# Performance work log

Hardware: AMD Instinct MI355X
Metric: run time of the kernel (lower is better)

## Reference

```python
import jax, jax.numpy as jnp
import numpy as np

LOSS_IDX = jnp.array([0, 1])    # loss_indices from __init__
BASIS_IDX = jnp.array([0, 1])   # dtw_mapping_basis (x, y)


def _dtw_path(cost):
    """Classic DTW DP + backtrack on cost [N, M].
    Returns padded alignment path (a, b) of length N+M-1 with validity mask.
    DP is run as an anti-diagonal wavefront scan (L = N+M-1 steps)."""
    N, M = cost.shape
    L = N + M - 1
    inf = jnp.float32(jnp.inf)
    i_idx = jnp.arange(N)

    def diag_step(carry, k):
        prev1, prev2 = carry  # diagonals k-1 and k-2, indexed by row i
        j = k - i_idx
        valid = (j >= 0) & (j < M)
        c = cost[i_idx, jnp.clip(j, 0, M - 1)]
        up = jnp.concatenate([jnp.full((1,), inf), prev1[:-1]])  # D[i-1, j]
        dg = jnp.concatenate([jnp.full((1,), inf), prev2[:-1]])  # D[i-1, j-1]
        lf = prev1                                               # D[i, j-1]
        best = jnp.minimum(jnp.minimum(up, dg), lf)
        best = jnp.where(jnp.isinf(best), jnp.float32(0.0), best)  # (0,0) seed
        cur = jnp.where(valid, c + best, inf)
        return (cur, prev1), cur

    init = (jnp.full((N,), inf), jnp.full((N,), inf))
    _, diags = jax.lax.scan(diag_step, init, jnp.arange(L))  # [L, N]: D[i,j] = diags[i+j, i]

    def getD(i, j):
        ok = (i >= 0) & (j >= 0)
        return jnp.where(ok, diags[jnp.clip(i + j, 0, L - 1), jnp.clip(i, 0, N - 1)], inf)

    def bt_step(carry, _):
        i, j, done = carry
        emit_valid = jnp.logical_not(done)
        cand = jnp.stack([getD(i - 1, j - 1), getD(i - 1, j), getD(i, j - 1)])
        m = jnp.argmin(cand)  # 0: diag, 1: up, 2: left
        ni = jnp.where(m == 2, i, i - 1)
        nj = jnp.where(m == 1, j, j - 1)
        done2 = done | ((i == 0) & (j == 0))
        ni = jnp.where(done2, 0, ni)
        nj = jnp.where(done2, 0, nj)
        return (ni, nj, done2), (i, j, emit_valid)

    init_bt = (jnp.int32(N - 1), jnp.int32(M - 1), jnp.bool_(False))
    _, (a, b, valid) = jax.lax.scan(bt_step, init_bt, None, length=L)
    return a, b, valid


def _dtw_loss_single(pred, targ, subcoef):
    # DTW alignment is computed on detached (numpy in torch) basis coords.
    p = jax.lax.stop_gradient(pred)[:, BASIS_IDX]
    t = jax.lax.stop_gradient(targ)[:, BASIS_IDX]
    # euclidean pairwise distance cost [N, M]
    cost = jnp.sqrt(jnp.sum((p[:, None, :] - t[None, :, :]) ** 2, axis=-1))
    a, b, valid = _dtw_path(cost)
    d = jnp.abs(pred[a][:, LOSS_IDX] - targ[b][:, LOSS_IDX]) * subcoef  # [L, 2]
    return jnp.sum(d * valid[:, None].astype(d.dtype))


def setup_inputs() -> dict:
    key = jax.random.key(0)
    k1, k2 = jax.random.split(key)
    B, N, M, F = 32, 1024, 1024, 4
    preds = jax.random.normal(k1, (B, N, F), dtype=jnp.float32)
    targs = jax.random.normal(k2, (B, M, F), dtype=jnp.float32)
    subcoef = jnp.ones((2,), dtype=jnp.float32)
    return {"preds": preds, "targs": targs, "subcoef": subcoef}


def reference(preds, targs, subcoef):
    per_sample = jax.vmap(_dtw_loss_single, in_axes=(0, 0, None))(preds, targs, subcoef)
    return jnp.sum(per_sample)
```

## Files before the change

kernel.cpp:

```cpp
#include <hip/hip_runtime.h>
#include <math.h>

#define BATCH 32
#define NN 1024
#define MM 1024
#define RR 4
#define CC 4
#define LANES 64
#define NWAVE 4
#define TPB (MM / 4)
#define NSUP (TPB + LANES - 1)
#define LAG 72
#define TOT (NSUP + (NWAVE - 1) * LAG)
#define DEPTH 32
#define DEC_WORDS_PER_BATCH ((NN / 4) * (MM / 4))
#define DEC_BYTES ((size_t)BATCH * DEC_WORDS_PER_BATCH * 4)
#define REQ_WS DEC_BYTES
#define LPATH (NN + MM - 1)

__global__ void init_kernel(float* out) { out[0] = 0.0f; }

__device__ inline void bt_walk4(const unsigned* __restrict__ sdec, int roff,
                                int iLow, int& i, int& j, int& n,
                                unsigned* __restrict__ path)
{
    int ri = i >> 2, jc = j >> 2;
    unsigned w = sdec[(ri - roff) * 256 + jc];
    while (true) {
        const int base = (ri - roff) * 256 + jc;
        const unsigned wl = sdec[(jc > 0)    ? base - 1   : base];
        const unsigned wu = sdec[(ri > roff) ? base - 256 : base];
        const unsigned wd = sdec[(ri > roff && jc > 0) ? base - 257 : base];
        bool done = false, susp = false;
        while (true) {
            path[n++] = ((unsigned)i << 16) | (unsigned)j;
            if ((i | j) == 0) { done = true; break; }
            const unsigned m = (w >> (((i & 3) * 4 + (j & 3)) * 2)) & 3u;
            i -= (m != 2u); j -= (m != 1u);
            if (i < iLow) { susp = true; break; }
            if ((i >> 2) != ri || (j >> 2) != jc) break;
        }
        if (done || susp) break;
        const int nri = i >> 2, njc = j >> 2;
        w = (nri == ri) ? wl : ((njc == jc) ? wu : wd);
        ri = nri; jc = njc;
    }
}

__global__ __launch_bounds__(256, 1) void dtw_fused(
    const float* __restrict__ preds, const float* __restrict__ targs,
    const float* __restrict__ subcoef, unsigned* __restrict__ dec,
    float* __restrict__ out)
{
    const int b = blockIdx.x, t = threadIdx.x;
    const int l = t & 63, w = t >> 6;
    const float INF = __builtin_inff();

    __shared__ float pxA[NN], pyA[NN], txA[MM], tyA[MM];
    __shared__ float4 ring[NWAVE - 1][DEPTH];
    __shared__ unsigned sdec[128 * 256];
    __shared__ unsigned path[LPATH + 1];
    __shared__ int sI, sJ, sN;
    __shared__ float wsum[NWAVE];

    for (int it = 0; it < NN / 256; ++it) {
        const int idx = it * 256 + t;
        const float4 p4 = ((const float4*)preds)[(size_t)b * NN + idx];
        pxA[idx] = p4.x; pyA[idx] = p4.y;
        const float4 t4 = ((const float4*)targs)[(size_t)b * MM + idx];
        txA[idx] = t4.x; tyA[idx] = t4.y;
    }
    __syncthreads();

    const int i0 = (w << 8) + (l << 2);
    const float4 px4 = ((const float4*)pxA)[i0 >> 2];
    const float4 py4 = ((const float4*)pyA)[i0 >> 2];
    const float px[RR] = {px4.x, px4.y, px4.z, px4.w};
    const float py[RR] = {py4.x, py4.y, py4.z, py4.w};
    unsigned* __restrict__ decT =
        dec + (size_t)b * DEC_WORDS_PER_BATCH + (size_t)(i0 >> 2) * TPB;

    float Dp[RR], Dbot[CC], bv[CC];
    #pragma unroll
    for (int r = 0; r < RR; ++r) Dp[r] = INF;
    #pragma unroll
    for (int c = 0; c < CC; ++c) { Dbot[c] = INF; bv[c] = INF; }
    float bndRet = (w == 0 && l == 0) ? 0.0f : INF;
    float4 gcur = make_float4(INF, INF, INF, INF);
    float4 tx4 = ((const float4*)txA)[0], ty4 = ((const float4*)tyA)[0];

    for (int u = 0; u < TOT; ++u) {
        const int ul = u - LAG * w;
        if (l == 0) {
            const bool gb = (w > 0) && (ul >= 0) && (ul < TPB);
            bv[0] = gb ? gcur.x : INF; bv[1] = gb ? gcur.y : INF;
            bv[2] = gb ? gcur.z : INF; bv[3] = gb ? gcur.w : INF;
        }
        const bool act = (ul >= l) && (ul < l + TPB);
        if (act) {
            const int j0 = CC * (ul - l);
            const float cx[CC] = {tx4.x, tx4.y, tx4.z, tx4.w};
            const float cy[CC] = {ty4.x, ty4.y, ty4.z, ty4.w};
            float cost[RR][CC];
            #pragma unroll
            for (int c = 0; c < CC; ++c)
                #pragma unroll
                for (int r = 0; r < RR; ++r) {
                    const float dx = px[r] - cx[c], dy = py[r] - cy[c];
                    cost[r][c] = __builtin_amdgcn_sqrtf(dx * dx + dy * dy);
                }
            unsigned word = 0;
            #pragma unroll
            for (int c = 0; c < CC; ++c) {
                float up = bv[c];
                float dg = (c == 0) ? bndRet : bv[c - 1];
                #pragma unroll
                for (int r = 0; r < RR; ++r) {
                    const float lf = Dp[r];
                    const unsigned m = (dg <= up && dg <= lf) ? 0u
                                     : ((up <= lf) ? 1u : 2u);
                    const float D = cost[r][c] + fminf(dg, fminf(up, lf));
                    word |= m << ((r * 4 + c) * 2);
                    dg = lf; up = D; Dp[r] = D;
                }
                Dbot[c] = up;
            }
            decT[j0 >> 2] = word;
            if (l == LANES - 1 && w < NWAVE - 1)
                ring[w][ul & (DEPTH - 1)] =
                    make_float4(Dbot[0], Dbot[1], Dbot[2], Dbot[3]);
        }
        bndRet = bv[CC - 1];
        #pragma unroll
        for (int c = 0; c < CC; ++c) bv[c] = __shfl_up(Dbot[c], 1);
        const int un = ul + 1;
        if (un >= l && un < l + TPB) {
            const int jn = CC * (un - l);
            tx4 = ((const float4*)txA)[jn >> 2];
            ty4 = ((const float4*)tyA)[jn >> 2];
        }
        if (l == 0 && w > 0 && un >= 0 && un < TPB)
            gcur = ring[w - 1][(un + 63) & (DEPTH - 1)];
        if ((u & 7) == 7) __syncthreads();
    }

    __threadfence_block();
    __syncthreads();

    const unsigned* __restrict__ decB = dec + (size_t)b * DEC_WORDS_PER_BATCH;
    {
        uint4* s4 = (uint4*)sdec;
        const uint4* g4 = (const uint4*)(decB + 128 * 256);
        for (int k = t; k < 8192; k += 256) s4[k] = g4[k];
    }
    __syncthreads();
    if (t == 0) {
        int i = NN - 1, j = MM - 1, n = 0;
        bt_walk4(sdec, 128, 512, i, j, n, path);
        sI = i; sJ = j; sN = n;
    }
    __syncthreads();
    {
        uint4* s4 = (uint4*)sdec;
        const uint4* g4 = (const uint4*)decB;
        for (int k = t; k < 8192; k += 256) s4[k] = g4[k];
    }
    __syncthreads();
    if (t == 0) {
        int i = sI, j = sJ, n = sN;
        bt_walk4(sdec, 0, 0, i, j, n, path);
        sN = n;
    }
    __syncthreads();

    const float sc0 = subcoef[0], sc1 = subcoef[1];
    const int n = sN;
    float acc = 0.0f;
    for (int p = t; p < n; p += 256) {
        const unsigned e = path[p];
        const int i = (int)(e >> 16), j = (int)(e & 0xffffu);
        acc += fabsf(pxA[i] - txA[j]) * sc0 + fabsf(pyA[i] - tyA[j]) * sc1;
    }
    #pragma unroll
    for (int o = 32; o > 0; o >>= 1) acc += __shfl_down(acc, o);
    if ((t & 63) == 0) wsum[t >> 6] = acc;
    __syncthreads();
    if (t == 0) atomicAdd(out, (wsum[0] + wsum[1]) + (wsum[2] + wsum[3]));
}

__global__ __launch_bounds__(256) void dtw_fallback(
    const float* __restrict__ preds, const float* __restrict__ targs,
    const float* __restrict__ subcoef, unsigned* __restrict__ dec,
    float* __restrict__ out)
{
    const int b = blockIdx.x;
    const int t = threadIdx.x;
    const float INF = __builtin_inff();
    __shared__ float px[NN], py[NN];
    __shared__ float txy[2 * MM];
    __shared__ float bbuf[2][256];

    for (int it = 0; it < NN / 256; ++it) {
        const int idx = it * 256 + t;
        const float4 p4 = ((const float4*)preds)[(size_t)b * NN + idx];
        px[idx] = p4.x; py[idx] = p4.y;
        const float4 t4 = ((const float4*)targs)[(size_t)b * MM + idx];
        txy[2 * idx] = t4.x; txy[2 * idx + 1] = t4.y;
    }
    bbuf[0][t] = INF; bbuf[1][t] = INF;
    __syncthreads();

    float pxr[4], pyr[4], Dp[4];
    #pragma unroll
    for (int r = 0; r < 4; ++r) {
        pxr[r] = px[4 * t + r]; pyr[r] = py[4 * t + r]; Dp[r] = INF;
    }
    float dgB = (t == 0) ? 0.0f : INF;
    unsigned packed = 0;
    unsigned* decB = dec + (size_t)b * 65536;
    for (int s = 0; s < MM + 255; ++s) {
        const int j = s - t;
        const float upB = (t == 0) ? INF : bbuf[(s + 1) & 1][t - 1];
        if (j >= 0 && j < MM) {
            const float txj = txy[2 * j], tyj = txy[2 * j + 1];
            float up = upB, dg = dgB;
            unsigned mbits = 0;
            #pragma unroll
            for (int r = 0; r < 4; ++r) {
                const float dx = pxr[r] - txj, dy = pyr[r] - tyj;
                const float c = sqrtf(dx * dx + dy * dy);
                const float lf = Dp[r];
                const unsigned m = (dg <= up && dg <= lf) ? 0u
                                 : ((up <= lf) ? 1u : 2u);
                mbits |= m << (r * 8 + (j & 3) * 2);
                const float Dc = c + fminf(up, fminf(dg, lf));
                dg = lf; up = Dc; Dp[r] = Dc;
            }
            packed |= mbits;
            if ((j & 3) == 3) { decB[(unsigned)t * 256 + (j >> 2)] = packed; packed = 0; }
            bbuf[s & 1][t] = Dp[3];
        }
        dgB = upB;
        __syncthreads();
    }
    __threadfence_block();
    __syncthreads();
    if (t == 0) {
        const float sc0 = subcoef[0], sc1 = subcoef[1];
        int i = NN - 1, jj = MM - 1;
        float loss = 0.0f;
        int ti = i >> 2, tj = jj >> 2;
        unsigned wv = decB[ti * 256 + tj];
        while (true) {
            const int tjl = (tj > 0) ? tj - 1 : 0;
            const int til = (ti > 0) ? ti - 1 : 0;
            const unsigned wl = decB[ti * 256 + tjl];
            const unsigned wu = decB[til * 256 + tj];
            const unsigned wd = decB[til * 256 + tjl];
            bool done = false;
            while (true) {
                loss += fabsf(px[i] - txy[2 * jj]) * sc0
                      + fabsf(py[i] - txy[2 * jj + 1]) * sc1;
                if ((i | jj) == 0) { done = true; break; }
                const unsigned m = (wv >> (((i & 3) * 4 + (jj & 3)) * 2)) & 3u;
                i -= (m != 2u); jj -= (m != 1u);
                if ((i >> 2) != ti || (jj >> 2) != tj) break;
            }
            if (done) break;
            const int nti = i >> 2, ntj = jj >> 2;
            wv = (nti == ti) ? wl : ((ntj == tj) ? wu : wd);
            ti = nti; tj = ntj;
        }
        atomicAdd(out, loss);
    }
}

extern "C" void kernel_launch(void* const* d_in, const int* in_sizes, int n_in,
                              void* d_out, int out_size, void* d_ws, size_t ws_size,
                              hipStream_t stream) {
    const float* preds   = (const float*)d_in[0];
    const float* targs   = (const float*)d_in[1];
    const float* subcoef = (const float*)d_in[2];
    float* out = (float*)d_out;
    unsigned* dec = (unsigned*)d_ws;

    init_kernel<<<1, 1, 0, stream>>>(out);
    if (ws_size >= REQ_WS) {
        dtw_fused<<<BATCH, 256, 0, stream>>>(preds, targs, subcoef, dec, out);
    } else {
        dtw_fallback<<<BATCH, 256, 0, stream>>>(preds, targs, subcoef, dec, out);
    }
}
```

Before: 597.1 us.

## Interleave two DP wavefront roles per wave in a 128-thread block

The block shrinks from four waves to two. Each wave now advances two independent row-band DP chains (roles w and w+2) in the same loop iteration, through a shared per-step helper. The aim is to expose instruction-level parallelism that hides the latency of the serial per-step dependency chain, including the cross-lane permute, which is now done with ds_bpermute instead of __shfl_up. The cost is that each SIMD now issues twice the instructions and holds twice the register state, and the final reduction and shared-memory copies are remapped to the smaller block.

```diff
diff --git a/kernel.cpp b/kernel.cpp
--- a/kernel.cpp
+++ b/kernel.cpp
@@ -47,7 +47,77 @@
     }
 }
 
-__global__ __launch_bounds__(256, 1) void dtw_fused(
+struct SS {
+    float Dp[RR], Dbot[CC], bv[CC], bndRet;
+    float px[RR], py[RR];
+    float4 tx4, ty4, gcur;
+    unsigned* decT;
+};
+
+__device__ __forceinline__ void dp_step(SS& S, const int u, const int role,
+                                        const int l, const int bpa,
+                                        const float* __restrict__ txA,
+                                        const float* __restrict__ tyA,
+                                        float4* __restrict__ ringW,
+                                        const float4* __restrict__ ringR)
+{
+    const float INF = __builtin_inff();
+    const int ul = u - LAG * role;
+    if (l == 0) {
+        const bool gb = (role > 0) && (ul >= 0) && (ul < TPB);
+        S.bv[0] = gb ? S.gcur.x : INF; S.bv[1] = gb ? S.gcur.y : INF;
+        S.bv[2] = gb ? S.gcur.z : INF; S.bv[3] = gb ? S.gcur.w : INF;
+    }
+    const bool act = (ul >= l) && (ul < l + TPB);
+    if (act) {
+        const int j0 = CC * (ul - l);
+        const float cx[CC] = {S.tx4.x, S.tx4.y, S.tx4.z, S.tx4.w};
+        const float cy[CC] = {S.ty4.x, S.ty4.y, S.ty4.z, S.ty4.w};
+        float cost[RR][CC];
+        #pragma unroll
+        for (int c = 0; c < CC; ++c)
+            #pragma unroll
+            for (int r = 0; r < RR; ++r) {
+                const float dx = S.px[r] - cx[c], dy = S.py[r] - cy[c];
+                cost[r][c] = __builtin_amdgcn_sqrtf(dx * dx + dy * dy);
+            }
+        unsigned word = 0;
+        #pragma unroll
+        for (int c = 0; c < CC; ++c) {
+            float up = S.bv[c];
+            float dg = (c == 0) ? S.bndRet : S.bv[c - 1];
+            #pragma unroll
+            for (int r = 0; r < RR; ++r) {
+                const float lf = S.Dp[r];
+                const unsigned m = (dg <= up && dg <= lf) ? 0u
+                                 : ((up <= lf) ? 1u : 2u);
+                const float D = cost[r][c] + fminf(dg, fminf(up, lf));
+                word |= m << ((r * 4 + c) * 2);
+                dg = lf; up = D; S.Dp[r] = D;
+            }
+            S.Dbot[c] = up;
+        }
+        S.decT[j0 >> 2] = word;
+        if (l == LANES - 1 && role < NWAVE - 1)
+            ringW[ul & (DEPTH - 1)] =
+                make_float4(S.Dbot[0], S.Dbot[1], S.Dbot[2], S.Dbot[3]);
+    }
+    S.bndRet = S.bv[CC - 1];
+    #pragma unroll
+    for (int c = 0; c < CC; ++c)
+        S.bv[c] = __int_as_float(
+            __builtin_amdgcn_ds_bpermute(bpa, __float_as_int(S.Dbot[c])));
+    const int un = ul + 1;
+    if (un >= l && un < l + TPB) {
+        const int jn = CC * (un - l);
+        S.tx4 = ((const float4*)txA)[jn >> 2];
+        S.ty4 = ((const float4*)tyA)[jn >> 2];
+    }
+    if (l == 0 && role > 0 && un >= 0 && un < TPB)
+        S.gcur = ringR[(un + 63) & (DEPTH - 1)];
+}
+
+__global__ __launch_bounds__(128, 1) void dtw_fused(
     const float* __restrict__ preds, const float* __restrict__ targs,
     const float* __restrict__ subcoef, unsigned* __restrict__ dec,
     float* __restrict__ out)
@@ -63,8 +133,8 @@
     __shared__ int sI, sJ, sN;
     __shared__ float wsum[NWAVE];
 
-    for (int it = 0; it < NN / 256; ++it) {
-        const int idx = it * 256 + t;
+    for (int it = 0; it < NN / 128; ++it) {
+        const int idx = it * 128 + t;
         const float4 p4 = ((const float4*)preds)[(size_t)b * NN + idx];
         pxA[idx] = p4.x; pyA[idx] = p4.y;
         const float4 t4 = ((const float4*)targs)[(size_t)b * MM + idx];
@@ -72,75 +142,45 @@
     }
     __syncthreads();
 
-    const int i0 = (w << 8) + (l << 2);
-    const float4 px4 = ((const float4*)pxA)[i0 >> 2];
-    const float4 py4 = ((const float4*)pyA)[i0 >> 2];
-    const float px[RR] = {px4.x, px4.y, px4.z, px4.w};
-    const float py[RR] = {py4.x, py4.y, py4.z, py4.w};
-    unsigned* __restrict__ decT =
-        dec + (size_t)b * DEC_WORDS_PER_BATCH + (size_t)(i0 >> 2) * TPB;
-
-    float Dp[RR], Dbot[CC], bv[CC];
-    #pragma unroll
-    for (int r = 0; r < RR; ++r) Dp[r] = INF;
-    #pragma unroll
-    for (int c = 0; c < CC; ++c) { Dbot[c] = INF; bv[c] = INF; }
-    float bndRet = (w == 0 && l == 0) ? 0.0f : INF;
-    float4 gcur = make_float4(INF, INF, INF, INF);
-    float4 tx4 = ((const float4*)txA)[0], ty4 = ((const float4*)tyA)[0];
+    const int bpa = (l - 1) << 2;
+    const int roleA = w, roleB = w + 2;
+    SS A, B;
+    {
+        const int i0a = (roleA << 8) + (l << 2);
+        const int i0b = (roleB << 8) + (l << 2);
+        const float4 pxa = ((const float4*)pxA)[i0a >> 2];
+        const float4 pya = ((const float4*)pyA)[i0a >> 2];
+        const float4 pxb = ((const float4*)pxA)[i0b >> 2];
+        const float4 pyb = ((const float4*)pyA)[i0b >> 2];
+        A.px[0] = pxa.x; A.px[1] = pxa.y; A.px[2] = pxa.z; A.px[3] = pxa.w;
+        A.py[0] = pya.x; A.py[1] = pya.y; A.py[2] = pya.z; A.py[3] = pya.w;
+        B.px[0] = pxb.x; B.px[1] = pxb.y; B.px[2] = pxb.z; B.px[3] = pxb.w;
+        B.py[0] = pyb.x; B.py[1] = pyb.y; B.py[2] = pyb.z; B.py[3] = pyb.w;
+        A.decT = dec + (size_t)b * DEC_WORDS_PER_BATCH + (size_t)(i0a >> 2) * TPB;
+        B.decT = dec + (size_t)b * DEC_WORDS_PER_BATCH + (size_t)(i0b >> 2) * TPB;
+    }
+    #pragma unroll
+    for (int r = 0; r < RR; ++r) { A.Dp[r] = INF; B.Dp[r] = INF; }
+    #pragma unroll
+    for (int c = 0; c < CC; ++c) {
+        A.Dbot[c] = INF; A.bv[c] = INF;
+        B.Dbot[c] = INF; B.bv[c] = INF;
+    }
+    A.bndRet = (roleA == 0 && l == 0) ? 0.0f : INF;
+    B.bndRet = INF;
+    A.gcur = make_float4(INF, INF, INF, INF);
+    B.gcur = make_float4(INF, INF, INF, INF);
+    A.tx4 = ((const float4*)txA)[0]; A.ty4 = ((const float4*)tyA)[0];
+    B.tx4 = ((const float4*)txA)[0]; B.ty4 = ((const float4*)tyA)[0];
+
+    float4* ringWA = ring[roleA];
+    const float4* ringRA = ring[(w > 0) ? (roleA - 1) : 0];
+    float4* ringWB = ring[(w == 0) ? 2 : 0];
+    const float4* ringRB = ring[roleB - 1];
 
     for (int u = 0; u < TOT; ++u) {
-        const int ul = u - LAG * w;
-        if (l == 0) {
-            const bool gb = (w > 0) && (ul >= 0) && (ul < TPB);
-            bv[0] = gb ? gcur.x : INF; bv[1] = gb ? gcur.y : INF;
-            bv[2] = gb ? gcur.z : INF; bv[3] = gb ? gcur.w : INF;
-        }
-        const bool act = (ul >= l) && (ul < l + TPB);
-        if (act) {
-            const int j0 = CC * (ul - l);
-            const float cx[CC] = {tx4.x, tx4.y, tx4.z, tx4.w};
-            const float cy[CC] = {ty4.x, ty4.y, ty4.z, ty4.w};
-            float cost[RR][CC];
-            #pragma unroll
-            for (int c = 0; c < CC; ++c)
-                #pragma unroll
-                for (int r = 0; r < RR; ++r) {
-                    const float dx = px[r] - cx[c], dy = py[r] - cy[c];
-                    cost[r][c] = __builtin_amdgcn_sqrtf(dx * dx + dy * dy);
-                }
-            unsigned word = 0;
-            #pragma unroll
-            for (int c = 0; c < CC; ++c) {
-                float up = bv[c];
-                float dg = (c == 0) ? bndRet : bv[c - 1];
-                #pragma unroll
-                for (int r = 0; r < RR; ++r) {
-                    const float lf = Dp[r];
-                    const unsigned m = (dg <= up && dg <= lf) ? 0u
-                                     : ((up <= lf) ? 1u : 2u);
-                    const float D = cost[r][c] + fminf(dg, fminf(up, lf));
-                    word |= m << ((r * 4 + c) * 2);
-                    dg = lf; up = D; Dp[r] = D;
-                }
-                Dbot[c] = up;
-            }
-            decT[j0 >> 2] = word;
-            if (l == LANES - 1 && w < NWAVE - 1)
-                ring[w][ul & (DEPTH - 1)] =
-                    make_float4(Dbot[0], Dbot[1], Dbot[2], Dbot[3]);
-        }
-        bndRet = bv[CC - 1];
-        #pragma unroll
-        for (int c = 0; c < CC; ++c) bv[c] = __shfl_up(Dbot[c], 1);
-        const int un = ul + 1;
-        if (un >= l && un < l + TPB) {
-            const int jn = CC * (un - l);
-            tx4 = ((const float4*)txA)[jn >> 2];
-            ty4 = ((const float4*)tyA)[jn >> 2];
-        }
-        if (l == 0 && w > 0 && un >= 0 && un < TPB)
-            gcur = ring[w - 1][(un + 63) & (DEPTH - 1)];
+        dp_step(A, u, roleA, l, bpa, txA, tyA, ringWA, ringRA);
+        dp_step(B, u, roleB, l, bpa, txA, tyA, ringWB, ringRB);
         if ((u & 7) == 7) __syncthreads();
     }
 
@@ -151,7 +191,7 @@
     {
         uint4* s4 = (uint4*)sdec;
         const uint4* g4 = (const uint4*)(decB + 128 * 256);
-        for (int k = t; k < 8192; k += 256) s4[k] = g4[k];
+        for (int k = t; k < 8192; k += 128) s4[k] = g4[k];
     }
     __syncthreads();
     if (t == 0) {
@@ -163,7 +203,7 @@
     {
         uint4* s4 = (uint4*)sdec;
         const uint4* g4 = (const uint4*)decB;
-        for (int k = t; k < 8192; k += 256) s4[k] = g4[k];
+        for (int k = t; k < 8192; k += 128) s4[k] = g4[k];
     }
     __syncthreads();
     if (t == 0) {
@@ -175,15 +215,19 @@
 
     const float sc0 = subcoef[0], sc1 = subcoef[1];
     const int n = sN;
-    float acc = 0.0f;
-    for (int p = t; p < n; p += 256) {
-        const unsigned e = path[p];
-        const int i = (int)(e >> 16), j = (int)(e & 0xffffu);
-        acc += fabsf(pxA[i] - txA[j]) * sc0 + fabsf(pyA[i] - tyA[j]) * sc1;
-    }
-    #pragma unroll
-    for (int o = 32; o > 0; o >>= 1) acc += __shfl_down(acc, o);
-    if ((t & 63) == 0) wsum[t >> 6] = acc;
+    #pragma unroll
+    for (int po = 0; po < 2; ++po) {
+        const int ow = 2 * w + po;
+        float acc = 0.0f;
+        for (int p = 64 * ow + l; p < n; p += 256) {
+            const unsigned e = path[p];
+            const int i = (int)(e >> 16), j = (int)(e & 0xffffu);
+            acc += fabsf(pxA[i] - txA[j]) * sc0 + fabsf(pyA[i] - tyA[j]) * sc1;
+        }
+        #pragma unroll
+        for (int o = 32; o > 0; o >>= 1) acc += __shfl_down(acc, o);
+        if (l == 0) wsum[ow] = acc;
+    }
     __syncthreads();
     if (t == 0) atomicAdd(out, (wsum[0] + wsum[1]) + (wsum[2] + wsum[3]));
 }
@@ -286,7 +330,7 @@
 
     init_kernel<<<1, 1, 0, stream>>>(out);
     if (ws_size >= REQ_WS) {
-        dtw_fused<<<BATCH, 256, 0, stream>>>(preds, targs, subcoef, dec, out);
+        dtw_fused<<<BATCH, 128, 0, stream>>>(preds, targs, subcoef, dec, out);
     } else {
         dtw_fallback<<<BATCH, 256, 0, stream>>>(preds, targs, subcoef, dec, out);
     }
```

Result: slower. 803.2 us (+34.5%).

## Store DTW decision words in wavefront-coalesced layout and unswizzle on load

Applied to the files above, without the earlier changes.

During the wavefront DP each lane used to write its decision word to a row-major address, so the 64 lanes of a wave wrote strided locations. The new layout indexes words by (wave, step mod 256, lane), so each wave's store per step is contiguous and coalesced. The backtrack staging now unswizzles into the old row-major shared layout, with scattered LDS writes and extra index arithmetic. All lanes now also read the ring buffer through a hoisted pointer, not just lane 0, which removes a lane branch but adds redundant LDS reads.

```diff
diff --git a/kernel.cpp b/kernel.cpp
--- a/kernel.cpp
+++ b/kernel.cpp
@@ -77,8 +77,8 @@
     const float4 py4 = ((const float4*)pyA)[i0 >> 2];
     const float px[RR] = {px4.x, px4.y, px4.z, px4.w};
     const float py[RR] = {py4.x, py4.y, py4.z, py4.w};
-    unsigned* __restrict__ decT =
-        dec + (size_t)b * DEC_WORDS_PER_BATCH + (size_t)(i0 >> 2) * TPB;
+    unsigned* __restrict__ decW =
+        dec + (size_t)b * DEC_WORDS_PER_BATCH + ((size_t)w << 14) + (size_t)l;
 
     float Dp[RR], Dbot[CC], bv[CC];
     #pragma unroll
@@ -88,6 +88,7 @@
     float bndRet = (w == 0 && l == 0) ? 0.0f : INF;
     float4 gcur = make_float4(INF, INF, INF, INF);
     float4 tx4 = ((const float4*)txA)[0], ty4 = ((const float4*)tyA)[0];
+    const float4* __restrict__ ringR = ring[(w > 0) ? (w - 1) : 0];
 
     for (int u = 0; u < TOT; ++u) {
         const int ul = u - LAG * w;
@@ -98,7 +99,6 @@
         }
         const bool act = (ul >= l) && (ul < l + TPB);
         if (act) {
-            const int j0 = CC * (ul - l);
             const float cx[CC] = {tx4.x, tx4.y, tx4.z, tx4.w};
             const float cy[CC] = {ty4.x, ty4.y, ty4.z, ty4.w};
             float cost[RR][CC];
@@ -125,7 +125,7 @@
                 }
                 Dbot[c] = up;
             }
-            decT[j0 >> 2] = word;
+            decW[(ul & 255) << 6] = word;
             if (l == LANES - 1 && w < NWAVE - 1)
                 ring[w][ul & (DEPTH - 1)] =
                     make_float4(Dbot[0], Dbot[1], Dbot[2], Dbot[3]);
@@ -139,8 +139,8 @@
             tx4 = ((const float4*)txA)[jn >> 2];
             ty4 = ((const float4*)tyA)[jn >> 2];
         }
-        if (l == 0 && w > 0 && un >= 0 && un < TPB)
-            gcur = ring[w - 1][(un + 63) & (DEPTH - 1)];
+        if (w > 0 && un >= 0 && un < TPB)
+            gcur = ringR[(un + 63) & (DEPTH - 1)];
         if ((u & 7) == 7) __syncthreads();
     }
 
@@ -149,9 +149,23 @@
 
     const unsigned* __restrict__ decB = dec + (size_t)b * DEC_WORDS_PER_BATCH;
     {
-        uint4* s4 = (uint4*)sdec;
-        const uint4* g4 = (const uint4*)(decB + 128 * 256);
-        for (int k = t; k < 8192; k += 256) s4[k] = g4[k];
+        const uint4* g4 = (const uint4*)(decB + 32768);
+        for (int k = t; k < 8192; k += 256) {
+            const uint4 v = g4[k];
+            const int kb = k << 2;
+            const int wv = kb >> 14;
+            const int rem = kb & 16383;
+            const int q = rem >> 6;
+            const int lb = rem & 63;
+            const unsigned wd[4] = {v.x, v.y, v.z, v.w};
+            #pragma unroll
+            for (int e = 0; e < 4; ++e) {
+                const int ll = lb + e;
+                const int row = (wv << 6) + ll;
+                const int jc = (q - ll) & 255;
+                sdec[(row << 8) + jc] = wd[e];
+            }
+        }
     }
     __syncthreads();
     if (t == 0) {
@@ -161,9 +175,23 @@
     }
     __syncthreads();
     {
-        uint4* s4 = (uint4*)sdec;
         const uint4* g4 = (const uint4*)decB;
-        for (int k = t; k < 8192; k += 256) s4[k] = g4[k];
+        for (int k = t; k < 8192; k += 256) {
+            const uint4 v = g4[k];
+            const int kb = k << 2;
+            const int wv = kb >> 14;
+            const int rem = kb & 16383;
+            const int q = rem >> 6;
+            const int lb = rem & 63;
+            const unsigned wd[4] = {v.x, v.y, v.z, v.w};
+            #pragma unroll
+            for (int e = 0; e < 4; ++e) {
+                const int ll = lb + e;
+                const int row = (wv << 6) + ll;
+                const int jc = (q - ll) & 255;
+                sdec[(row << 8) + jc] = wd[e];
+            }
+        }
     }
     __syncthreads();
     if (t == 0) {
```

New measurement: 608.9 us. Within noise of the previous version (+2.0%).

## Use single-wave 16x8 register tiles for the DTW wavefront and drop inter-wave ring

Applied to the files above, without the earlier changes.

Replaces the four-wave pipelined wavefront (4x4 tiles per lane, shared-memory ring hand-off and periodic block barriers) with a single 64-lane wave where each lane owns 16 rows and computes 8 columns per step. The number of serial wavefront steps falls from about 535 to 191 and the per-step __syncthreads disappears. Each lane now does 128 cells of dependent min/add per step, so the per-step critical path grows. The direction-word layout changes to column-major pairs so each lane writes two uint4 stores, and the backtrack addressing is updated to match. The shared-memory copies and the final reduction now run with only 64 threads.

```diff
diff --git a/kernel.cpp b/kernel.cpp
--- a/kernel.cpp
+++ b/kernel.cpp
@@ -4,15 +4,11 @@
 #define BATCH 32
 #define NN 1024
 #define MM 1024
-#define RR 4
-#define CC 4
+#define RR 16
+#define CC 8
 #define LANES 64
-#define NWAVE 4
-#define TPB (MM / 4)
-#define NSUP (TPB + LANES - 1)
-#define LAG 72
-#define TOT (NSUP + (NWAVE - 1) * LAG)
-#define DEPTH 32
+#define TPB (MM / CC)
+#define TOT (TPB + LANES - 1)
 #define DEC_WORDS_PER_BATCH ((NN / 4) * (MM / 4))
 #define DEC_BYTES ((size_t)BATCH * DEC_WORDS_PER_BATCH * 4)
 #define REQ_WS DEC_BYTES
@@ -20,17 +16,19 @@
 
 __global__ void init_kernel(float* out) { out[0] = 0.0f; }
 
-__device__ inline void bt_walk4(const unsigned* __restrict__ sdec, int roff,
+__device__ inline void bt_walkP(const unsigned* __restrict__ sdec, int riOff,
                                 int iLow, int& i, int& j, int& n,
                                 unsigned* __restrict__ path)
 {
     int ri = i >> 2, jc = j >> 2;
-    unsigned w = sdec[(ri - roff) * 256 + jc];
+#define WADDR(R, C) (((((C) >> 1)) << 8) + (((R) - riOff) << 1) + ((C) & 1))
+    unsigned w = sdec[WADDR(ri, jc)];
     while (true) {
-        const int base = (ri - roff) * 256 + jc;
-        const unsigned wl = sdec[(jc > 0)    ? base - 1   : base];
-        const unsigned wu = sdec[(ri > roff) ? base - 256 : base];
-        const unsigned wd = sdec[(ri > roff && jc > 0) ? base - 257 : base];
+        const int riu = (ri > riOff) ? ri - 1 : ri;
+        const int jcl = (jc > 0) ? jc - 1 : jc;
+        const unsigned wl = sdec[WADDR(ri, jcl)];
+        const unsigned wu = sdec[WADDR(riu, jc)];
+        const unsigned wd = sdec[WADDR(riu, jcl)];
         bool done = false, susp = false;
         while (true) {
             path[n++] = ((unsigned)i << 16) | (unsigned)j;
@@ -45,26 +43,24 @@
         w = (nri == ri) ? wl : ((njc == jc) ? wu : wd);
         ri = nri; jc = njc;
     }
-}
-
-__global__ __launch_bounds__(256, 1) void dtw_fused(
+#undef WADDR
+}
+
+__global__ __launch_bounds__(64, 1) void dtw_fused(
     const float* __restrict__ preds, const float* __restrict__ targs,
     const float* __restrict__ subcoef, unsigned* __restrict__ dec,
     float* __restrict__ out)
 {
-    const int b = blockIdx.x, t = threadIdx.x;
-    const int l = t & 63, w = t >> 6;
+    const int b = blockIdx.x, l = threadIdx.x;
     const float INF = __builtin_inff();
 
     __shared__ float pxA[NN], pyA[NN], txA[MM], tyA[MM];
-    __shared__ float4 ring[NWAVE - 1][DEPTH];
-    __shared__ unsigned sdec[128 * 256];
+    __shared__ unsigned sdec[32768];
     __shared__ unsigned path[LPATH + 1];
     __shared__ int sI, sJ, sN;
-    __shared__ float wsum[NWAVE];
-
-    for (int it = 0; it < NN / 256; ++it) {
-        const int idx = it * 256 + t;
+
+    for (int it = 0; it < NN / 64; ++it) {
+        const int idx = it * 64 + l;
         const float4 p4 = ((const float4*)preds)[(size_t)b * NN + idx];
         pxA[idx] = p4.x; pyA[idx] = p4.y;
         const float4 t4 = ((const float4*)targs)[(size_t)b * MM + idx];
@@ -72,76 +68,70 @@
     }
     __syncthreads();
 
-    const int i0 = (w << 8) + (l << 2);
-    const float4 px4 = ((const float4*)pxA)[i0 >> 2];
-    const float4 py4 = ((const float4*)pyA)[i0 >> 2];
-    const float px[RR] = {px4.x, px4.y, px4.z, px4.w};
-    const float py[RR] = {py4.x, py4.y, py4.z, py4.w};
-    unsigned* __restrict__ decT =
-        dec + (size_t)b * DEC_WORDS_PER_BATCH + (size_t)(i0 >> 2) * TPB;
-
-    float Dp[RR], Dbot[CC], bv[CC];
+    float px[RR], py[RR];
+    #pragma unroll
+    for (int k = 0; k < 4; ++k) {
+        const float4 p4 = ((const float4*)pxA)[4 * l + k];
+        px[4 * k] = p4.x; px[4 * k + 1] = p4.y; px[4 * k + 2] = p4.z; px[4 * k + 3] = p4.w;
+        const float4 q4 = ((const float4*)pyA)[4 * l + k];
+        py[4 * k] = q4.x; py[4 * k + 1] = q4.y; py[4 * k + 2] = q4.z; py[4 * k + 3] = q4.w;
+    }
+    unsigned* __restrict__ decW = dec + (size_t)b * DEC_WORDS_PER_BATCH
+                                + ((size_t)(l >> 5) << 15) + ((size_t)(l & 31) << 3);
+
+    float Dp[RR], bv[CC], bot[CC];
     #pragma unroll
     for (int r = 0; r < RR; ++r) Dp[r] = INF;
     #pragma unroll
-    for (int c = 0; c < CC; ++c) { Dbot[c] = INF; bv[c] = INF; }
-    float bndRet = (w == 0 && l == 0) ? 0.0f : INF;
-    float4 gcur = make_float4(INF, INF, INF, INF);
-    float4 tx4 = ((const float4*)txA)[0], ty4 = ((const float4*)tyA)[0];
-
+    for (int c = 0; c < CC; ++c) { bv[c] = INF; bot[c] = INF; }
+    float bndRet = (l == 0) ? 0.0f : INF;
+    float4 tx0 = ((const float4*)txA)[0], tx1 = ((const float4*)txA)[1];
+    float4 ty0 = ((const float4*)tyA)[0], ty1 = ((const float4*)tyA)[1];
+
+    #pragma unroll 1
     for (int u = 0; u < TOT; ++u) {
-        const int ul = u - LAG * w;
-        if (l == 0) {
-            const bool gb = (w > 0) && (ul >= 0) && (ul < TPB);
-            bv[0] = gb ? gcur.x : INF; bv[1] = gb ? gcur.y : INF;
-            bv[2] = gb ? gcur.z : INF; bv[3] = gb ? gcur.w : INF;
-        }
-        const bool act = (ul >= l) && (ul < l + TPB);
+        const int q = u - l;
+        const bool act = (q >= 0) && (q < TPB);
         if (act) {
-            const int j0 = CC * (ul - l);
-            const float cx[CC] = {tx4.x, tx4.y, tx4.z, tx4.w};
-            const float cy[CC] = {ty4.x, ty4.y, ty4.z, ty4.w};
-            float cost[RR][CC];
-            #pragma unroll
-            for (int c = 0; c < CC; ++c)
-                #pragma unroll
-                for (int r = 0; r < RR; ++r) {
-                    const float dx = px[r] - cx[c], dy = py[r] - cy[c];
-                    cost[r][c] = __builtin_amdgcn_sqrtf(dx * dx + dy * dy);
-                }
-            unsigned word = 0;
+            const float cx[CC] = {tx0.x, tx0.y, tx0.z, tx0.w,
+                                  tx1.x, tx1.y, tx1.z, tx1.w};
+            const float cy[CC] = {ty0.x, ty0.y, ty0.z, ty0.w,
+                                  ty1.x, ty1.y, ty1.z, ty1.w};
+            unsigned wd[8] = {0, 0, 0, 0, 0, 0, 0, 0};
             #pragma unroll
             for (int c = 0; c < CC; ++c) {
                 float up = bv[c];
                 float dg = (c == 0) ? bndRet : bv[c - 1];
                 #pragma unroll
                 for (int r = 0; r < RR; ++r) {
+                    const float dx = px[r] - cx[c], dy = py[r] - cy[c];
+                    const float cost = __builtin_amdgcn_sqrtf(dx * dx + dy * dy);
                     const float lf = Dp[r];
-                    const unsigned m = (dg <= up && dg <= lf) ? 0u
-                                     : ((up <= lf) ? 1u : 2u);
-                    const float D = cost[r][c] + fminf(dg, fminf(up, lf));
-                    word |= m << ((r * 4 + c) * 2);
+                    const float mn = fminf(dg, fminf(up, lf));
+                    const unsigned m = (mn == dg) ? 0u : ((mn == up) ? 1u : 2u);
+                    wd[(r >> 2) * 2 + (c >> 2)] |= m << (((r & 3) * 4 + (c & 3)) * 2);
+                    const float D = cost + mn;
                     dg = lf; up = D; Dp[r] = D;
                 }
-                Dbot[c] = up;
+                bot[c] = up;
             }
-            decT[j0 >> 2] = word;
-            if (l == LANES - 1 && w < NWAVE - 1)
-                ring[w][ul & (DEPTH - 1)] =
-                    make_float4(Dbot[0], Dbot[1], Dbot[2], Dbot[3]);
+            uint4* dst = (uint4*)(decW + ((size_t)q << 8));
+            dst[0] = make_uint4(wd[0], wd[1], wd[2], wd[3]);
+            dst[1] = make_uint4(wd[4], wd[5], wd[6], wd[7]);
         }
         bndRet = bv[CC - 1];
         #pragma unroll
-        for (int c = 0; c < CC; ++c) bv[c] = __shfl_up(Dbot[c], 1);
-        const int un = ul + 1;
-        if (un >= l && un < l + TPB) {
-            const int jn = CC * (un - l);
-            tx4 = ((const float4*)txA)[jn >> 2];
-            ty4 = ((const float4*)tyA)[jn >> 2];
-        }
-        if (l == 0 && w > 0 && un >= 0 && un < TPB)
-            gcur = ring[w - 1][(un + 63) & (DEPTH - 1)];
-        if ((u & 7) == 7) __syncthreads();
+        for (int c = 0; c < CC; ++c) {
+            bv[c] = __shfl_up(bot[c], 1);
+            if (l == 0) bv[c] = INF;
+        }
+        const int qn = u + 1 - l;
+        if (qn >= 0 && qn < TPB) {
+            tx0 = ((const float4*)txA)[2 * qn];
+            tx1 = ((const float4*)txA)[2 * qn + 1];
+            ty0 = ((const float4*)tyA)[2 * qn];
+            ty1 = ((const float4*)tyA)[2 * qn + 1];
+        }
     }
 
     __threadfence_block();
@@ -149,26 +139,26 @@
 
     const unsigned* __restrict__ decB = dec + (size_t)b * DEC_WORDS_PER_BATCH;
     {
+        const uint4* g4 = (const uint4*)(decB + 32768);
         uint4* s4 = (uint4*)sdec;
-        const uint4* g4 = (const uint4*)(decB + 128 * 256);
-        for (int k = t; k < 8192; k += 256) s4[k] = g4[k];
-    }
-    __syncthreads();
-    if (t == 0) {
+        for (int k = l; k < 8192; k += 64) s4[k] = g4[k];
+    }
+    __syncthreads();
+    if (l == 0) {
         int i = NN - 1, j = MM - 1, n = 0;
-        bt_walk4(sdec, 128, 512, i, j, n, path);
+        bt_walkP(sdec, 128, 512, i, j, n, path);
         sI = i; sJ = j; sN = n;
     }
     __syncthreads();
     {
+        const uint4* g4 = (const uint4*)decB;
         uint4* s4 = (uint4*)sdec;
-        const uint4* g4 = (const uint4*)decB;
-        for (int k = t; k < 8192; k += 256) s4[k] = g4[k];
-    }
-    __syncthreads();
-    if (t == 0) {
+        for (int k = l; k < 8192; k += 64) s4[k] = g4[k];
+    }
+    __syncthreads();
+    if (l == 0) {
         int i = sI, j = sJ, n = sN;
-        bt_walk4(sdec, 0, 0, i, j, n, path);
+        bt_walkP(sdec, 0, 0, i, j, n, path);
         sN = n;
     }
     __syncthreads();
@@ -176,16 +166,14 @@
     const float sc0 = subcoef[0], sc1 = subcoef[1];
     const int n = sN;
     float acc = 0.0f;
-    for (int p = t; p < n; p += 256) {
+    for (int p = l; p < n; p += 64) {
         const unsigned e = path[p];
         const int i = (int)(e >> 16), j = (int)(e & 0xffffu);
         acc += fabsf(pxA[i] - txA[j]) * sc0 + fabsf(pyA[i] - tyA[j]) * sc1;
     }
     #pragma unroll
     for (int o = 32; o > 0; o >>= 1) acc += __shfl_down(acc, o);
-    if ((t & 63) == 0) wsum[t >> 6] = acc;
-    __syncthreads();
-    if (t == 0) atomicAdd(out, (wsum[0] + wsum[1]) + (wsum[2] + wsum[3]));
+    if (l == 0) atomicAdd(out, acc);
 }
 
 __global__ __launch_bounds__(256) void dtw_fallback(
@@ -286,7 +274,7 @@
 
     init_kernel<<<1, 1, 0, stream>>>(out);
     if (ws_size >= REQ_WS) {
-        dtw_fused<<<BATCH, 256, 0, stream>>>(preds, targs, subcoef, dec, out);
+        dtw_fused<<<BATCH, 64, 0, stream>>>(preds, targs, subcoef, dec, out);
     } else {
         dtw_fallback<<<BATCH, 256, 0, stream>>>(preds, targs, subcoef, dec, out);
     }
```

Result: slower. 982.6 us (+64.6%).
